# Optimization experiments

Hardware: AMD Instinct MI355X
Metric: run time of the kernel (lower is better)

The kernel has to match this reference:

```python
import jax, jax.numpy as jnp
import numpy as np


def setup_inputs() -> dict:
    key = jax.random.key(0)
    k1, k2, k3, k4 = jax.random.split(key, 4)
    B, T, C, H = 32, 2048, 384, 64
    x = jax.random.normal(k1, (B, T, C), dtype=jnp.float32)
    # nn.Linear(C, H, bias=False): weight stored [H, C], applied as x @ W.T.
    # We store the transposed [C, H] form directly.
    s = 1.0 / np.sqrt(C)
    Wk = jax.random.normal(k2, (C, H), dtype=jnp.float32) * s
    Wq = jax.random.normal(k3, (C, H), dtype=jnp.float32) * s
    Wv = jax.random.normal(k4, (C, H), dtype=jnp.float32) * s
    return {"x": x, "Wk": Wk, "Wq": Wq, "Wv": Wv}


def reference(x, Wk, Wq, Wv):
    # x: [B, T, C]; Wk/Wq/Wv: [C, H]
    T = x.shape[1]
    H = Wk.shape[1]
    k = jnp.einsum('btc,ch->bth', x, Wk)
    q = jnp.einsum('btc,ch->bth', x, Wq)
    v = jnp.einsum('btc,ch->bth', x, Wv)
    scale = H ** (-0.5)
    scores = jnp.einsum('bth,bsh->bts', q, k) * scale  # [B, T, T]
    causal = jnp.tril(jnp.ones((T, T), dtype=bool))
    scores = jnp.where(causal, scores, -jnp.inf)
    attn = jax.nn.softmax(scores, axis=-1)
    # dropout is identity in eval mode
    out = jnp.einsum('bts,bsh->bth', attn, v)  # [B, T, H]
    return out
```

## Files before the change

### kernel.cpp

```cpp
#include <hip/hip_runtime.h>

typedef __bf16 bf16_8 __attribute__((ext_vector_type(8)));
typedef __bf16 bf16_4 __attribute__((ext_vector_type(4)));
typedef float  f32x4  __attribute__((ext_vector_type(4)));

#define NB 32
#define NT 2048
#define NC 384
#define NH 64

static __device__ __forceinline__ f32x4 mfma16(bf16_8 a, bf16_8 b, f32x4 c) {
  return __builtin_amdgcn_mfma_f32_16x16x32_bf16(a, b, c, 0, 0, 0);
}

__global__ void pack_w_kernel(const float* __restrict__ Wk, const float* __restrict__ Wq,
                              const float* __restrict__ Wv, __bf16* __restrict__ Wt) {
  int idx = blockIdx.x * 256 + threadIdx.x;
  if (idx >= 192 * NC) return;
  int n = idx / NC, k = idx % NC;
  int sel = n >> 6, h = n & 63;
  const float* W = (sel == 0) ? Wq : (sel == 1 ? Wk : Wv);
  float v = W[k * NH + h];
  if (sel == 0) v *= 0.125f;
  Wt[idx] = (__bf16)v;
}

__launch_bounds__(1024, 4)
__global__ void qkv_kernel(const float* __restrict__ x, const __bf16* __restrict__ Wt,
                           __bf16* __restrict__ Q, __bf16* __restrict__ K,
                           __bf16* __restrict__ Vt) {
  __shared__ __bf16 Wl[192 * 384];

  const int tid  = threadIdx.x;
  const int lane = tid & 63, wq = tid >> 6;
  const int quad = lane >> 4, l16 = lane & 15;
  const int rowblk = blockIdx.x * 256;
  const int rbase  = rowblk + wq * 16;
  const int row    = rbase + l16;

  #pragma unroll
  for (int i = 0; i < 9; ++i) {
    int g = tid + i * 1024;
    int r = g / 48, c = g - r * 48;
    int p = c ^ (r & 7);
    uint4 v = ((const uint4*)Wt)[g];
    *(uint4*)&Wl[(r * 48 + p) * 8] = v;
  }
  __syncthreads();

  f32x4 acc[12];
  #pragma unroll
  for (int n = 0; n < 12; ++n) acc[n] = f32x4{0.f, 0.f, 0.f, 0.f};

  const float* xrow = x + (size_t)row * NC;
  f32x4 x0 = *(const f32x4*)(xrow + quad * 8);
  f32x4 x1 = *(const f32x4*)(xrow + quad * 8 + 4);

  #pragma unroll
  for (int kc = 0; kc < 12; ++kc) {
    f32x4 nx0, nx1;
    if (kc < 11) {
      const float* xp = xrow + (kc + 1) * 32 + quad * 8;
      nx0 = *(const f32x4*)xp;
      nx1 = *(const f32x4*)(xp + 4);
    }
    bf16_8 a;
    a[0] = (__bf16)x0[0]; a[1] = (__bf16)x0[1]; a[2] = (__bf16)x0[2]; a[3] = (__bf16)x0[3];
    a[4] = (__bf16)x1[0]; a[5] = (__bf16)x1[1]; a[6] = (__bf16)x1[2]; a[7] = (__bf16)x1[3];
    const int pc = (kc * 4 + quad) ^ (l16 & 7);
    const int cbase = l16 * 48 + pc;
    #pragma unroll
    for (int n = 0; n < 12; ++n) {
      bf16_8 b = *(const bf16_8*)&Wl[(n * 16 * 48 + cbase) * 8];
      acc[n] = mfma16(a, b, acc[n]);
    }
    x0 = nx0; x1 = nx1;
  }

  #pragma unroll
  for (int n = 0; n < 8; ++n)
    #pragma unroll
    for (int r = 0; r < 4; ++r) {
      int orow = rbase + quad * 4 + r;
      int h = (n & 3) * 16 + l16;
      __bf16 bv = (__bf16)acc[n][r];
      if (n < 4) Q[(size_t)orow * NH + h] = bv;
      else       K[(size_t)orow * NH + h] = bv;
    }

  __syncthreads();
  __bf16 (*Vl)[264] = (__bf16(*)[264])Wl;
  #pragma unroll
  for (int n = 8; n < 12; ++n) {
    int h = (n - 8) * 16 + l16;
    int t0 = wq * 16 + quad * 4;
    bf16_4 p;
    p[0] = (__bf16)acc[n][0]; p[1] = (__bf16)acc[n][1];
    p[2] = (__bf16)acc[n][2]; p[3] = (__bf16)acc[n][3];
    *(bf16_4*)&Vl[h][t0] = p;
  }
  __syncthreads();
  {
    int h = tid >> 4, seg = tid & 15;
    int bb = rowblk >> 11, t0 = (rowblk & (NT - 1)) + seg * 16;
    const __bf16* src = &Vl[h][seg * 16];
    __bf16* dst = Vt + ((size_t)(bb * NH + h)) * NT + t0;
    ((uint4*)dst)[0] = ((const uint4*)src)[0];
    ((uint4*)dst)[1] = ((const uint4*)src)[1];
  }
}

__launch_bounds__(256)
__global__ void attn_kernel(const __bf16* __restrict__ Q, const __bf16* __restrict__ K,
                            const __bf16* __restrict__ Vt, float* __restrict__ out) {
  __shared__ __bf16 Ks[2][64][72];
  __shared__ __bf16 Vs[2][64][72];
  __shared__ __bf16 Ps[4][16][72];

  const int tid  = threadIdx.x;
  const int lane = tid & 63, wq = tid >> 6;
  const int quad = lane >> 4, l16 = lane & 15;
  const int b    = blockIdx.x >> 4;
  const int pair = blockIdx.x & 15;

  const float NEG_INF = -__builtin_inff();
  const int r = tid >> 2, seg = tid & 3;
  const __bf16* Kg = K  + (size_t)b * NT * NH;
  const __bf16* Vg = Vt + (size_t)b * NH * NT;

  for (int pass = 0; pass < 2; ++pass) {
    const int qt = pass ? pair : (31 - pair);
    const int q0 = qt * 64;
    const int nIter = qt + 1;

    const __bf16* qrow = Q + ((size_t)(b * NT + q0 + wq * 16 + l16)) * NH + quad * 8;
    bf16_8 qf0 = *(const bf16_8*)qrow;
    bf16_8 qf1 = *(const bf16_8*)(qrow + 32);

    f32x4 o[4];
    #pragma unroll
    for (int i = 0; i < 4; ++i) o[i] = f32x4{0.f, 0.f, 0.f, 0.f};
    float m_i = NEG_INF, l_i = 0.f;

    __syncthreads();

    {
      const uint4* sK = (const uint4*)(Kg + (size_t)r * NH + seg * 16);
      uint4 ka = sK[0], kb = sK[1];
      const uint4* sV = (const uint4*)(Vg + (size_t)r * NT + seg * 16);
      uint4 va = sV[0], vb = sV[1];
      *(uint4*)&Ks[0][r][seg * 16]     = ka;
      *(uint4*)&Ks[0][r][seg * 16 + 8] = kb;
      *(uint4*)&Vs[0][r][seg * 16]     = va;
      *(uint4*)&Vs[0][r][seg * 16 + 8] = vb;
    }

    for (int i = 0; i < nIter; ++i) {
      const int cur = i & 1;
      const bool more = (i + 1 < nIter);
      uint4 nka, nkb, nva, nvb;
      if (more) {
        const int s0n = (i + 1) * 64;
        const uint4* sK = (const uint4*)(Kg + (size_t)(s0n + r) * NH + seg * 16);
        nka = sK[0]; nkb = sK[1];
        const uint4* sV = (const uint4*)(Vg + (size_t)r * NT + s0n + seg * 16);
        nva = sV[0]; nvb = sV[1];
      }
      __syncthreads();

      f32x4 s[4];
      #pragma unroll
      for (int st = 0; st < 4; ++st) {
        bf16_8 a0 = *(const bf16_8*)&Ks[cur][st * 16 + l16][quad * 8];
        bf16_8 a1 = *(const bf16_8*)&Ks[cur][st * 16 + l16][quad * 8 + 32];
        f32x4 accv = f32x4{0.f, 0.f, 0.f, 0.f};
        accv = mfma16(a0, qf0, accv);
        accv = mfma16(a1, qf1, accv);
        s[st] = accv;
      }

      if (i == qt) {
        int qg = wq * 16 + l16;
        #pragma unroll
        for (int st = 0; st < 4; ++st)
          #pragma unroll
          for (int rr = 0; rr < 4; ++rr) {
            int sg = st * 16 + quad * 4 + rr;
            if (sg > qg) s[st][rr] = NEG_INF;
          }
      }

      float mx = NEG_INF;
      #pragma unroll
      for (int st = 0; st < 4; ++st)
        #pragma unroll
        for (int rr = 0; rr < 4; ++rr) mx = fmaxf(mx, s[st][rr]);
      mx = fmaxf(mx, __shfl_xor(mx, 16));
      mx = fmaxf(mx, __shfl_xor(mx, 32));
      float m_new = fmaxf(m_i, mx);
      float alpha = __expf(m_i - m_new);

      float lsum = 0.f;
      #pragma unroll
      for (int st = 0; st < 4; ++st) {
        bf16_4 pk;
        #pragma unroll
        for (int rr = 0; rr < 4; ++rr) {
          float p = __expf(s[st][rr] - m_new);
          lsum += p;
          pk[rr] = (__bf16)p;
        }
        *(bf16_4*)&Ps[wq][l16][st * 16 + quad * 4] = pk;
      }
      lsum += __shfl_xor(lsum, 16);
      lsum += __shfl_xor(lsum, 32);
      l_i = l_i * alpha + lsum;
      m_i = m_new;

      f32x4 av;
      #pragma unroll
      for (int rr = 0; rr < 4; ++rr) av[rr] = __shfl(alpha, quad * 4 + rr);
      #pragma unroll
      for (int nt = 0; nt < 4; ++nt)
        #pragma unroll
        for (int rr = 0; rr < 4; ++rr) o[nt][rr] *= av[rr];

      bf16_8 pa0 = *(const bf16_8*)&Ps[wq][l16][quad * 8];
      bf16_8 pa1 = *(const bf16_8*)&Ps[wq][l16][quad * 8 + 32];
      #pragma unroll
      for (int nt = 0; nt < 4; ++nt) {
        bf16_8 b0 = *(const bf16_8*)&Vs[cur][nt * 16 + l16][quad * 8];
        bf16_8 b1 = *(const bf16_8*)&Vs[cur][nt * 16 + l16][quad * 8 + 32];
        o[nt] = mfma16(pa0, b0, o[nt]);
        o[nt] = mfma16(pa1, b1, o[nt]);
      }

      if (more) {
        *(uint4*)&Ks[1 - cur][r][seg * 16]     = nka;
        *(uint4*)&Ks[1 - cur][r][seg * 16 + 8] = nkb;
        *(uint4*)&Vs[1 - cur][r][seg * 16]     = nva;
        *(uint4*)&Vs[1 - cur][r][seg * 16 + 8] = nvb;
      }
    }

    f32x4 lv;
    #pragma unroll
    for (int rr = 0; rr < 4; ++rr) lv[rr] = 1.f / __shfl(l_i, quad * 4 + rr);
    float* op = out + ((size_t)(b * NT + q0 + wq * 16 + quad * 4)) * NH + l16;
    #pragma unroll
    for (int nt = 0; nt < 4; ++nt)
      #pragma unroll
      for (int rr = 0; rr < 4; ++rr)
        op[(size_t)rr * NH + nt * 16] = o[nt][rr] * lv[rr];
  }
}

extern "C" void kernel_launch(void* const* d_in, const int* in_sizes, int n_in,
                              void* d_out, int out_size, void* d_ws, size_t ws_size,
                              hipStream_t stream) {
  const float* x  = (const float*)d_in[0];
  const float* Wk = (const float*)d_in[1];
  const float* Wq = (const float*)d_in[2];
  const float* Wv = (const float*)d_in[3];
  float* out = (float*)d_out;

  char* ws = (char*)d_ws;
  __bf16* Wt  = (__bf16*)ws;
  __bf16* Qb  = (__bf16*)(ws + 256 * 1024);
  __bf16* Kb  = Qb + (size_t)NB * NT * NH;
  __bf16* Vtb = Kb + (size_t)NB * NT * NH;

  pack_w_kernel<<<288, 256, 0, stream>>>(Wk, Wq, Wv, Wt);
  qkv_kernel<<<256, 1024, 0, stream>>>(x, Wt, Qb, Kb, Vtb);
  attn_kernel<<<NB * 16, 256, 0, stream>>>(Qb, Kb, Vtb, out);
}
```

Before: 209.7 us.

## Use 128-key super-tiles in attention, exp2 softmax, deeper x prefetch in QKV

The attention kernel now processes 128 keys per iteration with a single-buffered K/V tile and register prefetch. This halves the number of loop iterations, barriers and softmax rescales, at the cost of an extra barrier per iteration and lost double buffering. Softmax switches to exp2 by folding log2(e) into the Q weight scale. The QKV projection prefetches x four chunks ahead instead of one. Masking still handles the partial last super-tile.

Measured after the change: 257.7 us. 22.9% more time.

```diff
diff --git a/kernel.cpp b/kernel.cpp
--- a/kernel.cpp
+++ b/kernel.cpp
@@ -21,7 +21,7 @@
   int sel = n >> 6, h = n & 63;
   const float* W = (sel == 0) ? Wq : (sel == 1 ? Wk : Wv);
   float v = W[k * NH + h];
-  if (sel == 0) v *= 0.125f;
+  if (sel == 0) v *= 0.125f * 1.44269504088896f;
   Wt[idx] = (__bf16)v;
 }
 
@@ -53,20 +53,26 @@
   for (int n = 0; n < 12; ++n) acc[n] = f32x4{0.f, 0.f, 0.f, 0.f};
 
   const float* xrow = x + (size_t)row * NC;
-  f32x4 x0 = *(const f32x4*)(xrow + quad * 8);
-  f32x4 x1 = *(const f32x4*)(xrow + quad * 8 + 4);
+  f32x4 xp0[4], xp1[4];
+  #pragma unroll
+  for (int d = 0; d < 4; ++d) {
+    xp0[d] = *(const f32x4*)(xrow + d * 32 + quad * 8);
+    xp1[d] = *(const f32x4*)(xrow + d * 32 + quad * 8 + 4);
+  }
 
   #pragma unroll
   for (int kc = 0; kc < 12; ++kc) {
-    f32x4 nx0, nx1;
-    if (kc < 11) {
-      const float* xp = xrow + (kc + 1) * 32 + quad * 8;
-      nx0 = *(const f32x4*)xp;
-      nx1 = *(const f32x4*)(xp + 4);
-    }
+    const int slot = kc & 3;
     bf16_8 a;
-    a[0] = (__bf16)x0[0]; a[1] = (__bf16)x0[1]; a[2] = (__bf16)x0[2]; a[3] = (__bf16)x0[3];
-    a[4] = (__bf16)x1[0]; a[5] = (__bf16)x1[1]; a[6] = (__bf16)x1[2]; a[7] = (__bf16)x1[3];
+    a[0] = (__bf16)xp0[slot][0]; a[1] = (__bf16)xp0[slot][1];
+    a[2] = (__bf16)xp0[slot][2]; a[3] = (__bf16)xp0[slot][3];
+    a[4] = (__bf16)xp1[slot][0]; a[5] = (__bf16)xp1[slot][1];
+    a[6] = (__bf16)xp1[slot][2]; a[7] = (__bf16)xp1[slot][3];
+    if (kc + 4 < 12) {
+      const float* xp = xrow + (kc + 4) * 32 + quad * 8;
+      xp0[slot] = *(const f32x4*)xp;
+      xp1[slot] = *(const f32x4*)(xp + 4);
+    }
     const int pc = (kc * 4 + quad) ^ (l16 & 7);
     const int cbase = l16 * 48 + pc;
     #pragma unroll
@@ -74,7 +80,6 @@
       bf16_8 b = *(const bf16_8*)&Wl[(n * 16 * 48 + cbase) * 8];
       acc[n] = mfma16(a, b, acc[n]);
     }
-    x0 = nx0; x1 = nx1;
   }
 
   #pragma unroll
@@ -110,12 +115,12 @@
   }
 }
 
-__launch_bounds__(256)
+__launch_bounds__(256, 2)
 __global__ void attn_kernel(const __bf16* __restrict__ Q, const __bf16* __restrict__ K,
                             const __bf16* __restrict__ Vt, float* __restrict__ out) {
-  __shared__ __bf16 Ks[2][64][72];
-  __shared__ __bf16 Vs[2][64][72];
-  __shared__ __bf16 Ps[4][16][72];
+  __shared__ __bf16 Ks[128][72];
+  __shared__ __bf16 Vs[64][136];
+  __shared__ __bf16 Ps[4][16][136];
 
   const int tid  = threadIdx.x;
   const int lane = tid & 63, wq = tid >> 6;
@@ -124,14 +129,15 @@
   const int pair = blockIdx.x & 15;
 
   const float NEG_INF = -__builtin_inff();
-  const int r = tid >> 2, seg = tid & 3;
+  const int kr = tid >> 1, kc4 = (tid & 1) * 32;
+  const int vr = tid >> 2, vc  = (tid & 3) * 32;
   const __bf16* Kg = K  + (size_t)b * NT * NH;
   const __bf16* Vg = Vt + (size_t)b * NH * NT;
 
   for (int pass = 0; pass < 2; ++pass) {
     const int qt = pass ? pair : (31 - pair);
     const int q0 = qt * 64;
-    const int nIter = qt + 1;
+    const int nSuper = (qt + 2) >> 1;
 
     const __bf16* qrow = Q + ((size_t)(b * NT + q0 + wq * 16 + l16)) * NH + quad * 8;
     bf16_8 qf0 = *(const bf16_8*)qrow;
@@ -142,75 +148,72 @@
     for (int i = 0; i < 4; ++i) o[i] = f32x4{0.f, 0.f, 0.f, 0.f};
     float m_i = NEG_INF, l_i = 0.f;
 
-    __syncthreads();
-
     {
-      const uint4* sK = (const uint4*)(Kg + (size_t)r * NH + seg * 16);
-      uint4 ka = sK[0], kb = sK[1];
-      const uint4* sV = (const uint4*)(Vg + (size_t)r * NT + seg * 16);
-      uint4 va = sV[0], vb = sV[1];
-      *(uint4*)&Ks[0][r][seg * 16]     = ka;
-      *(uint4*)&Ks[0][r][seg * 16 + 8] = kb;
-      *(uint4*)&Vs[0][r][seg * 16]     = va;
-      *(uint4*)&Vs[0][r][seg * 16 + 8] = vb;
-    }
-
-    for (int i = 0; i < nIter; ++i) {
-      const int cur = i & 1;
-      const bool more = (i + 1 < nIter);
-      uint4 nka, nkb, nva, nvb;
+      const uint4* kp = (const uint4*)(Kg + (size_t)kr * NH + kc4);
+      const uint4* vp = (const uint4*)(Vg + (size_t)vr * NT + vc);
+      uint4 pk0 = kp[0], pk1 = kp[1], pk2 = kp[2], pk3 = kp[3];
+      uint4 pv0 = vp[0], pv1 = vp[1], pv2 = vp[2], pv3 = vp[3];
+      *(uint4*)&Ks[kr][kc4]      = pk0; *(uint4*)&Ks[kr][kc4 + 8]  = pk1;
+      *(uint4*)&Ks[kr][kc4 + 16] = pk2; *(uint4*)&Ks[kr][kc4 + 24] = pk3;
+      *(uint4*)&Vs[vr][vc]       = pv0; *(uint4*)&Vs[vr][vc + 8]   = pv1;
+      *(uint4*)&Vs[vr][vc + 16]  = pv2; *(uint4*)&Vs[vr][vc + 24]  = pv3;
+    }
+
+    for (int i = 0; i < nSuper; ++i) {
+      const bool more = (i + 1 < nSuper);
+      uint4 pk[4], pv[4];
       if (more) {
-        const int s0n = (i + 1) * 64;
-        const uint4* sK = (const uint4*)(Kg + (size_t)(s0n + r) * NH + seg * 16);
-        nka = sK[0]; nkb = sK[1];
-        const uint4* sV = (const uint4*)(Vg + (size_t)r * NT + s0n + seg * 16);
-        nva = sV[0]; nvb = sV[1];
+        const int s0n = (i + 1) * 128;
+        const uint4* kp = (const uint4*)(Kg + (size_t)(s0n + kr) * NH + kc4);
+        pk[0] = kp[0]; pk[1] = kp[1]; pk[2] = kp[2]; pk[3] = kp[3];
+        const uint4* vp = (const uint4*)(Vg + (size_t)vr * NT + s0n + vc);
+        pv[0] = vp[0]; pv[1] = vp[1]; pv[2] = vp[2]; pv[3] = vp[3];
       }
       __syncthreads();
 
-      f32x4 s[4];
-      #pragma unroll
-      for (int st = 0; st < 4; ++st) {
-        bf16_8 a0 = *(const bf16_8*)&Ks[cur][st * 16 + l16][quad * 8];
-        bf16_8 a1 = *(const bf16_8*)&Ks[cur][st * 16 + l16][quad * 8 + 32];
+      f32x4 sv[8];
+      #pragma unroll
+      for (int st = 0; st < 8; ++st) {
+        bf16_8 a0 = *(const bf16_8*)&Ks[st * 16 + l16][quad * 8];
+        bf16_8 a1 = *(const bf16_8*)&Ks[st * 16 + l16][quad * 8 + 32];
         f32x4 accv = f32x4{0.f, 0.f, 0.f, 0.f};
         accv = mfma16(a0, qf0, accv);
         accv = mfma16(a1, qf1, accv);
-        s[st] = accv;
-      }
-
-      if (i == qt) {
-        int qg = wq * 16 + l16;
-        #pragma unroll
-        for (int st = 0; st < 4; ++st)
+        sv[st] = accv;
+      }
+
+      if (i == nSuper - 1) {
+        int slimit = q0 + wq * 16 + l16 - i * 128;
+        #pragma unroll
+        for (int st = 0; st < 8; ++st)
           #pragma unroll
           for (int rr = 0; rr < 4; ++rr) {
-            int sg = st * 16 + quad * 4 + rr;
-            if (sg > qg) s[st][rr] = NEG_INF;
+            int sloc = st * 16 + quad * 4 + rr;
+            if (sloc > slimit) sv[st][rr] = NEG_INF;
           }
       }
 
       float mx = NEG_INF;
       #pragma unroll
-      for (int st = 0; st < 4; ++st)
-        #pragma unroll
-        for (int rr = 0; rr < 4; ++rr) mx = fmaxf(mx, s[st][rr]);
+      for (int st = 0; st < 8; ++st)
+        #pragma unroll
+        for (int rr = 0; rr < 4; ++rr) mx = fmaxf(mx, sv[st][rr]);
       mx = fmaxf(mx, __shfl_xor(mx, 16));
       mx = fmaxf(mx, __shfl_xor(mx, 32));
       float m_new = fmaxf(m_i, mx);
-      float alpha = __expf(m_i - m_new);
+      float alpha = __builtin_amdgcn_exp2f(m_i - m_new);
 
       float lsum = 0.f;
       #pragma unroll
-      for (int st = 0; st < 4; ++st) {
-        bf16_4 pk;
+      for (int st = 0; st < 8; ++st) {
+        bf16_4 pkv;
         #pragma unroll
         for (int rr = 0; rr < 4; ++rr) {
-          float p = __expf(s[st][rr] - m_new);
+          float p = __builtin_amdgcn_exp2f(sv[st][rr] - m_new);
           lsum += p;
-          pk[rr] = (__bf16)p;
+          pkv[rr] = (__bf16)p;
         }
-        *(bf16_4*)&Ps[wq][l16][st * 16 + quad * 4] = pk;
+        *(bf16_4*)&Ps[wq][l16][st * 16 + quad * 4] = pkv;
       }
       lsum += __shfl_xor(lsum, 16);
       lsum += __shfl_xor(lsum, 32);
@@ -225,21 +228,25 @@
         #pragma unroll
         for (int rr = 0; rr < 4; ++rr) o[nt][rr] *= av[rr];
 
-      bf16_8 pa0 = *(const bf16_8*)&Ps[wq][l16][quad * 8];
-      bf16_8 pa1 = *(const bf16_8*)&Ps[wq][l16][quad * 8 + 32];
+      bf16_8 pa[4];
+      #pragma unroll
+      for (int c = 0; c < 4; ++c)
+        pa[c] = *(const bf16_8*)&Ps[wq][l16][c * 32 + quad * 8];
       #pragma unroll
       for (int nt = 0; nt < 4; ++nt) {
-        bf16_8 b0 = *(const bf16_8*)&Vs[cur][nt * 16 + l16][quad * 8];
-        bf16_8 b1 = *(const bf16_8*)&Vs[cur][nt * 16 + l16][quad * 8 + 32];
-        o[nt] = mfma16(pa0, b0, o[nt]);
-        o[nt] = mfma16(pa1, b1, o[nt]);
-      }
-
+        #pragma unroll
+        for (int c = 0; c < 4; ++c) {
+          bf16_8 bv = *(const bf16_8*)&Vs[nt * 16 + l16][c * 32 + quad * 8];
+          o[nt] = mfma16(pa[c], bv, o[nt]);
+        }
+      }
+
+      __syncthreads();
       if (more) {
-        *(uint4*)&Ks[1 - cur][r][seg * 16]     = nka;
-        *(uint4*)&Ks[1 - cur][r][seg * 16 + 8] = nkb;
-        *(uint4*)&Vs[1 - cur][r][seg * 16]     = nva;
-        *(uint4*)&Vs[1 - cur][r][seg * 16 + 8] = nvb;
+        *(uint4*)&Ks[kr][kc4]      = pk[0]; *(uint4*)&Ks[kr][kc4 + 8]  = pk[1];
+        *(uint4*)&Ks[kr][kc4 + 16] = pk[2]; *(uint4*)&Ks[kr][kc4 + 24] = pk[3];
+        *(uint4*)&Vs[vr][vc]       = pv[0]; *(uint4*)&Vs[vr][vc + 8]   = pv[1];
+        *(uint4*)&Vs[vr][vc + 16]  = pv[2]; *(uint4*)&Vs[vr][vc + 24]  = pv[3];
       }
     }
 
```
